# Optimization experiments

Measured on AMD Instinct MI355X. Metric: run time of the kernel, lower is better.

Reference implementation:

```python
import jax, jax.numpy as jnp
import numpy as np

B, T, D, H = 256, 512, 512, 512


def setup_inputs() -> dict:
    key = jax.random.key(0)
    k1, k2, k3, k4 = jax.random.split(key, 4)
    inputs = jax.random.normal(k1, (B, T, D), dtype=jnp.float32)
    lengths = jax.random.randint(k2, (B,), 0, T).astype(jnp.int32)
    # LSTM params. Flax nn.LSTMCell uses per-gate dense layers:
    #  input dense (with bias) and recurrent dense (no bias). Packing the
    #  four gates (i, f, g, o) into one matrix is mathematically identical.
    Wx = jax.random.normal(k3, (D, 4 * H), dtype=jnp.float32) * (1.0 / np.sqrt(D))
    Wh = jax.random.normal(k4, (H, 4 * H), dtype=jnp.float32) * (1.0 / np.sqrt(H))
    b = jnp.zeros((4 * H,), dtype=jnp.float32)
    return {"inputs": inputs, "lengths": lengths, "Wx": Wx, "Wh": Wh, "b": b}


def reference(inputs, lengths, Wx, Wh, b):
    batch = inputs.shape[0]
    hidden = Wh.shape[0]
    x_tbd = jnp.swapaxes(inputs, 0, 1)  # [T, B, D]

    def step(carry, x_t):
        c, h = carry
        # fused gate pre-activations: [B, 4H]
        z = x_t @ Wx + h @ Wh + b
        i, f, g, o = jnp.split(z, 4, axis=-1)
        i = jax.nn.sigmoid(i)
        f = jax.nn.sigmoid(f)
        g = jnp.tanh(g)
        o = jax.nn.sigmoid(o)
        c_new = f * c + i * g
        h_new = o * jnp.tanh(c_new)
        return (c_new, h_new), h_new

    c0 = jnp.zeros((batch, hidden), dtype=inputs.dtype)
    h0 = jnp.zeros((batch, hidden), dtype=inputs.dtype)
    _, hs = jax.lax.scan(step, (c0, h0), x_tbd)  # hs: [T, B, H]

    # select output at last valid timestep per example
    idx = jnp.maximum(0, lengths - 1)  # [B]
    return hs[idx, jnp.arange(batch), :]  # [B, H]
```

## Files before the change

### kernel.cpp

```cpp
#include <hip/hip_runtime.h>

#define Bb 256
#define Tt 512
#define Dd 512
#define Hh 512
#define KTOT 1024
#define FOURH 2048

typedef __attribute__((ext_vector_type(8))) short bf16x8;
typedef __attribute__((ext_vector_type(4))) float f32x4;

__device__ __forceinline__ unsigned short f2bf(float f) {
    union { float f; unsigned u; } x; x.f = f;
    unsigned u = x.u;
    unsigned r = u + 0x7FFFu + ((u >> 16) & 1u);
    return (unsigned short)(r >> 16);
}
__device__ __forceinline__ float bf2f(unsigned short s) {
    union { unsigned u; float f; } x; x.u = ((unsigned)s) << 16;
    return x.f;
}

__device__ __forceinline__ uint4 load16_sc0(const void* p) {
    uint4 v;
    asm volatile("global_load_dwordx4 %0, %1, off sc0" : "=v"(v) : "v"(p));
    return v;
}
__device__ __forceinline__ uint4 load16_sc01(const void* p) {
    uint4 v;
    asm volatile("global_load_dwordx4 %0, %1, off sc0 sc1" : "=v"(v) : "v"(p));
    return v;
}

__global__ void prep_w(const float* __restrict__ Wx, const float* __restrict__ Wh,
                       unsigned short* __restrict__ WT_hi, unsigned short* __restrict__ WT_lo) {
    __shared__ float tile[32][33];
    int n0 = (blockIdx.x & 63) * 32;
    int k0 = (blockIdx.x >> 6) * 32;
    int tx = threadIdx.x & 31;
    int ty = threadIdx.x >> 5;
    for (int q = 0; q < 4; ++q) {
        int k = k0 + ty + q * 8;
        int n = n0 + tx;
        float v = (k < Dd) ? Wx[(size_t)k * FOURH + n] : Wh[(size_t)(k - Dd) * FOURH + n];
        tile[ty + q * 8][tx] = v;
    }
    __syncthreads();
    for (int q = 0; q < 4; ++q) {
        int nl = ty + q * 8;
        int kl = tx;
        float v = tile[kl][nl];
        unsigned short hi = f2bf(v);
        unsigned short lo = f2bf(v - bf2f(hi));
        size_t o = (size_t)(n0 + nl) * KTOT + (size_t)(k0 + kl);
        WT_hi[o] = hi;
        WT_lo[o] = lo;
    }
}

__global__ void init_state(float* __restrict__ c_st,
                           unsigned short* __restrict__ h_bufs,
                           unsigned int* __restrict__ ctrl) {
    int i = blockIdx.x * blockDim.x + threadIdx.x;
    if (i < Bb * Hh) {
        c_st[i] = 0.f;
        for (int q = 0; q < 4; ++q)
            h_bufs[(size_t)q * Bb * Hh + i] = 0;
    }
    if (i < 272) ctrl[i] = 0u;
}

__global__ __launch_bounds__(512) void lstm_persist5(
    const float* __restrict__ X, const int* __restrict__ lengths,
    const unsigned short* __restrict__ WT_hi, const unsigned short* __restrict__ WT_lo,
    const float* __restrict__ bias,
    unsigned short* __restrict__ h_base,
    unsigned int* __restrict__ ctrl,
    float* __restrict__ out)
{
    __shared__ unsigned short HLDS[32768];
    __shared__ unsigned short XLDS[32768];
    __shared__ float zbuf[8][32][17];
    __shared__ int sgrp, sslt, smix;

    const int tid = threadIdx.x;
    const int w8 = tid >> 6;
    const int lane = tid & 63;
    const int l15 = lane & 15;
    const int q4 = lane >> 4;
    const int klo = q4 * 8;

    unsigned xcc;
    asm volatile("s_getreg_b32 %0, hwreg(HW_REG_XCC_ID, 0, 4)" : "=s"(xcc));
    xcc &= 7u;

    unsigned int* pool = ctrl + 256;
    unsigned int* rcnt = ctrl + 264;

    if (tid == 0) {
        unsigned my = __hip_atomic_fetch_add(&pool[xcc], 1u, __ATOMIC_RELAXED, __HIP_MEMORY_SCOPE_SYSTEM);
        asm volatile("s_waitcnt vmcnt(0)" ::: "memory");
        __hip_atomic_fetch_add(rcnt, 1u, __ATOMIC_RELAXED, __HIP_MEMORY_SCOPE_SYSTEM);
        while (__hip_atomic_load(rcnt, __ATOMIC_RELAXED, __HIP_MEMORY_SCOPE_SYSTEM) < 256u)
            __builtin_amdgcn_s_sleep(2);
        unsigned cl[8];
        for (int g = 0; g < 8; ++g)
            cl[g] = __hip_atomic_load(&pool[g], __ATOMIC_RELAXED, __HIP_MEMORY_SCOPE_SYSTEM);
        int group = 0, slot = 0;
        if (my < 32u) { group = (int)xcc; slot = (int)my; }
        else {
            int r = (int)my - 32;
            for (int g = 0; g < (int)xcc; ++g) { int e = (int)cl[g] - 32; if (e > 0) r += e; }
            for (int g = 0; g < 8; ++g) {
                int def = 32 - (int)cl[g];
                if (def <= 0) continue;
                if (r < def) { group = g; slot = (int)cl[g] + r; break; }
                r -= def;
            }
        }
        sgrp = group; sslt = slot; smix = (cl[group] < 32u) ? 1 : 0;
    }
    __syncthreads();
    const int group = sgrp;
    const int slot = sslt;
    const int mixed = smix;

    const int r0 = group * 32;
    const int j0 = slot * 16;
    const int gate = w8 & 3;
    const int khalf = w8 >> 2;

    const size_t HB = (size_t)Bb * Hh;
    unsigned short* h_hi0 = h_base;
    unsigned short* h_lo0 = h_base + HB;
    unsigned short* h_hi1 = h_base + 2 * HB;
    unsigned short* h_lo1 = h_base + 3 * HB;

    const int colg = gate * 512 + j0 + l15;
    const size_t bbase = (size_t)colg * KTOT + (size_t)khalf * 512;
    const unsigned short* bhp = &WT_hi[bbase];
    const unsigned short* blp = &WT_lo[bbase];

    const int xr = tid >> 4;
    const int xk0 = (tid & 15) * 32;
    const float* xbase = &X[((size_t)(r0 + xr) * Tt) * Dd + xk0];

    const int er = tid >> 4;
    const int ej = tid & 15;
    const int row_g = r0 + er;
    const int col_h = j0 + ej;
    const size_t oidx = (size_t)row_g * Hh + col_h;
    int oT = lengths[row_g] - 1; if (oT < 0) oT = 0;
    const float b0 = bias[col_h], b1 = bias[512 + col_h],
                b2 = bias[1024 + col_h], b3 = bias[1536 + col_h];
    float creg = 0.f;

    unsigned int* mycnt = &ctrl[group * 32];

    for (int t = 0; t < Tt; ++t) {
        const unsigned short* hrh = (t & 1) ? h_hi1 : h_hi0;
        const unsigned short* hrl = (t & 1) ? h_lo1 : h_lo0;
        unsigned short* hwh = (t & 1) ? h_hi0 : h_hi1;
        unsigned short* hwl = (t & 1) ? h_lo0 : h_lo1;

        float4 xv[8];
        const float* xp = xbase + (size_t)t * Dd;
#pragma unroll
        for (int i = 0; i < 8; ++i) xv[i] = ((const float4*)xp)[i];

        uint4 hv[8];
        const unsigned short* hsliceh = hrh + (size_t)r0 * Hh;
        const unsigned short* hslicel = hrl + (size_t)r0 * Hh;
        if (!mixed) {
#pragma unroll
            for (int i = 0; i < 8; ++i) {
                const int c = i * 512 + tid;
                const unsigned short* src = ((c >> 11) ? hslicel : hsliceh) + (c & 2047) * 8;
                hv[i] = load16_sc0(src);
            }
        } else {
#pragma unroll
            for (int i = 0; i < 8; ++i) {
                const int c = i * 512 + tid;
                const unsigned short* src = ((c >> 11) ? hslicel : hsliceh) + (c & 2047) * 8;
                hv[i] = load16_sc01(src);
            }
        }
        asm volatile("s_waitcnt vmcnt(0)" ::: "memory");
        __builtin_amdgcn_sched_barrier(0);

#pragma unroll
        for (int i = 0; i < 8; ++i) {
            const int c = i * 512 + tid;
            const int arr = c >> 11, cc = c & 2047;
            const int row = cc >> 6, k8 = cc & 63;
            const int mi = row >> 4, lr = row & 15, ks = k8 >> 2, qq = k8 & 3;
            *(uint4*)&HLDS[((size_t)((arr * 2 + mi) * 16 + ks) * 64 + (qq * 16 + lr)) * 8] = hv[i];
        }
#pragma unroll
        for (int c2 = 0; c2 < 4; ++c2) {
            float vv[8];
            *(float4*)&vv[0] = xv[2 * c2];
            *(float4*)&vv[4] = xv[2 * c2 + 1];
            bf16x8 hv8, lv8;
#pragma unroll
            for (int e = 0; e < 8; ++e) {
                unsigned short hs = f2bf(vv[e]);
                hv8[e] = (short)hs;
                lv8[e] = (short)f2bf(vv[e] - bf2f(hs));
            }
            const int k = xk0 + c2 * 8;
            const int mi = xr >> 4, lr = xr & 15, ks = k >> 5, qq = (k >> 3) & 3;
            const int lidx = ((mi * 16 + ks) * 64 + (qq * 16 + lr)) * 8;
            *(bf16x8*)&XLDS[lidx] = hv8;
            *(bf16x8*)&XLDS[lidx + 16384] = lv8;
        }
        __syncthreads();

        const unsigned short* ALDS = khalf ? HLDS : XLDS;
        f32x4 acc[2][3];
#pragma unroll
        for (int mi = 0; mi < 2; ++mi)
#pragma unroll
            for (int s = 0; s < 3; ++s)
                acc[mi][s] = (f32x4){0.f, 0.f, 0.f, 0.f};

#pragma unroll
        for (int ks = 0; ks < 16; ++ks) {
            const int kk = ks * 32 + klo;
            const bf16x8 bh = *(const bf16x8*)&bhp[kk];
            const bf16x8 bl = *(const bf16x8*)&blp[kk];
#pragma unroll
            for (int mi = 0; mi < 2; ++mi) {
                const bf16x8 ah = *(const bf16x8*)&ALDS[((mi * 16 + ks) * 64 + lane) * 8];
                const bf16x8 al = *(const bf16x8*)&ALDS[(((2 + mi) * 16 + ks) * 64 + lane) * 8];
                acc[mi][0] = __builtin_amdgcn_mfma_f32_16x16x32_bf16(ah, bh, acc[mi][0], 0, 0, 0);
                acc[mi][1] = __builtin_amdgcn_mfma_f32_16x16x32_bf16(ah, bl, acc[mi][1], 0, 0, 0);
                acc[mi][2] = __builtin_amdgcn_mfma_f32_16x16x32_bf16(al, bh, acc[mi][2], 0, 0, 0);
            }
        }

#pragma unroll
        for (int mi = 0; mi < 2; ++mi) {
            const f32x4 z = acc[mi][0] + acc[mi][1] + acc[mi][2];
#pragma unroll
            for (int r = 0; r < 4; ++r)
                zbuf[w8][mi * 16 + q4 * 4 + r][l15] = z[r];
        }
        __syncthreads();

        float zi = zbuf[0][er][ej] + zbuf[4][er][ej] + b0;
        float zf = zbuf[1][er][ej] + zbuf[5][er][ej] + b1;
        float zg = zbuf[2][er][ej] + zbuf[6][er][ej] + b2;
        float zo = zbuf[3][er][ej] + zbuf[7][er][ej] + b3;
        float ig = 1.f / (1.f + expf(-zi));
        float fg = 1.f / (1.f + expf(-zf));
        float gg = tanhf(zg);
        float og = 1.f / (1.f + expf(-zo));
        float cn = fg * creg + ig * gg;
        creg = cn;
        float hn = og * tanhf(cn);
        unsigned short hh = f2bf(hn);
        unsigned short hl = f2bf(hn - bf2f(hh));
        if (!mixed) {
            hwh[oidx] = hh;
            hwl[oidx] = hl;
        } else {
            __hip_atomic_store(&hwh[oidx], hh, __ATOMIC_RELAXED, __HIP_MEMORY_SCOPE_SYSTEM);
            __hip_atomic_store(&hwl[oidx], hl, __ATOMIC_RELAXED, __HIP_MEMORY_SCOPE_SYSTEM);
        }
        if (t == oT) out[oidx] = hn;

        if (t < Tt - 1) {
            __syncthreads();
            if (tid == 0) {
                __hip_atomic_fetch_add(mycnt, 1u, __ATOMIC_RELAXED, __HIP_MEMORY_SCOPE_SYSTEM);
                const unsigned int target = (unsigned int)(t + 1) * 32u;
                while (__hip_atomic_load(mycnt, __ATOMIC_RELAXED, __HIP_MEMORY_SCOPE_SYSTEM) < target)
                    __builtin_amdgcn_s_sleep(2);
            }
            __syncthreads();
        }
    }
}

__global__ __launch_bounds__(512) void lstm_step4(
    const float* __restrict__ X, const int* __restrict__ lengths,
    const unsigned short* __restrict__ WT_hi, const unsigned short* __restrict__ WT_lo,
    const float* __restrict__ bias,
    float* __restrict__ c_st,
    const unsigned short* __restrict__ h_r_hi, const unsigned short* __restrict__ h_r_lo,
    unsigned short* __restrict__ h_w_hi, unsigned short* __restrict__ h_w_lo,
    float* __restrict__ out, int t)
{
    __shared__ float zbuf[8][16][17];

    const int bx = blockIdx.x;
    const int xcd = bx & 7;
    const int rem = bx >> 3;
    const int m0 = (rem & 15) * 16;
    const int col_group = xcd * 4 + (rem >> 4);
    const int hc0 = col_group * 16;
    const int tid = threadIdx.x;
    const int w8 = tid >> 6;
    const int lane = tid & 63;
    const int gate = w8 & 3;
    const int khalf = w8 >> 2;

    f32x4 ahh = (f32x4){0,0,0,0}, ahl = (f32x4){0,0,0,0}, alh = (f32x4){0,0,0,0};

    const int colk = gate * 512 + hc0 + (lane & 15);
    const size_t bbase = (size_t)colk * KTOT;
    const int klo = (lane >> 4) * 8;
    const int row = m0 + (lane & 15);

    if (khalf == 0) {
        const float* xrow = &X[((size_t)row * Tt + t) * Dd];
        const unsigned short* bhp = &WT_hi[bbase];
        const unsigned short* blp = &WT_lo[bbase];
#pragma unroll
        for (int ks = 0; ks < 16; ++ks) {
            const int kk = ks * 32 + klo;
            const float4 v0 = *(const float4*)&xrow[kk];
            const float4 v1 = *(const float4*)&xrow[kk + 4];
            float vv[8] = {v0.x, v0.y, v0.z, v0.w, v1.x, v1.y, v1.z, v1.w};
            bf16x8 ah, al;
#pragma unroll
            for (int e = 0; e < 8; ++e) {
                unsigned short hi = f2bf(vv[e]);
                ah[e] = (short)hi;
                al[e] = (short)f2bf(vv[e] - bf2f(hi));
            }
            const bf16x8 bh = *(const bf16x8*)&bhp[kk];
            const bf16x8 bl = *(const bf16x8*)&blp[kk];
            ahh = __builtin_amdgcn_mfma_f32_16x16x32_bf16(ah, bh, ahh, 0, 0, 0);
            ahl = __builtin_amdgcn_mfma_f32_16x16x32_bf16(ah, bl, ahl, 0, 0, 0);
            alh = __builtin_amdgcn_mfma_f32_16x16x32_bf16(al, bh, alh, 0, 0, 0);
        }
    } else {
        const unsigned short* hrh = &h_r_hi[(size_t)row * Hh];
        const unsigned short* hrl = &h_r_lo[(size_t)row * Hh];
        const unsigned short* bhp = &WT_hi[bbase + 512];
        const unsigned short* blp = &WT_lo[bbase + 512];
#pragma unroll
        for (int ks = 0; ks < 16; ++ks) {
            const int kk = ks * 32 + klo;
            const bf16x8 ah = *(const bf16x8*)&hrh[kk];
            const bf16x8 al = *(const bf16x8*)&hrl[kk];
            const bf16x8 bh = *(const bf16x8*)&bhp[kk];
            const bf16x8 bl = *(const bf16x8*)&blp[kk];
            ahh = __builtin_amdgcn_mfma_f32_16x16x32_bf16(ah, bh, ahh, 0, 0, 0);
            ahl = __builtin_amdgcn_mfma_f32_16x16x32_bf16(ah, bl, ahl, 0, 0, 0);
            alh = __builtin_amdgcn_mfma_f32_16x16x32_bf16(al, bh, alh, 0, 0, 0);
        }
    }

    const f32x4 z = ahh + ahl + alh;
#pragma unroll
    for (int r = 0; r < 4; ++r)
        zbuf[w8][(lane >> 4) * 4 + r][lane & 15] = z[r];
    __syncthreads();

    if (tid < 256) {
        const int r = tid >> 4;
        const int j = tid & 15;
        const int row_g = m0 + r;
        const int col_g = hc0 + j;
        float zi = zbuf[0][r][j] + zbuf[4][r][j] + bias[col_g];
        float zf = zbuf[1][r][j] + zbuf[5][r][j] + bias[512 + col_g];
        float zg = zbuf[2][r][j] + zbuf[6][r][j] + bias[1024 + col_g];
        float zo = zbuf[3][r][j] + zbuf[7][r][j] + bias[1536 + col_g];
        float ig = 1.f / (1.f + expf(-zi));
        float fg = 1.f / (1.f + expf(-zf));
        float gg = tanhf(zg);
        float og = 1.f / (1.f + expf(-zo));
        const size_t idx = (size_t)row_g * Hh + col_g;
        float cn = fg * c_st[idx] + ig * gg;
        float hn = og * tanhf(cn);
        c_st[idx] = cn;
        unsigned short hh = f2bf(hn);
        h_w_hi[idx] = hh;
        h_w_lo[idx] = f2bf(hn - bf2f(hh));
        int len = lengths[row_g];
        int oidx = len - 1; if (oidx < 0) oidx = 0;
        if (t == oidx) out[idx] = hn;
    }
}

extern "C" void kernel_launch(void* const* d_in, const int* in_sizes, int n_in,
                              void* d_out, int out_size, void* d_ws, size_t ws_size,
                              hipStream_t stream) {
    const float* X = (const float*)d_in[0];
    const int* lengths = (const int*)d_in[1];
    const float* Wx = (const float*)d_in[2];
    const float* Wh = (const float*)d_in[3];
    const float* bias = (const float*)d_in[4];
    float* out = (float*)d_out;

    char* ws = (char*)d_ws;
    unsigned short* WT_hi = (unsigned short*)ws;
    unsigned short* WT_lo = (unsigned short*)(ws + (4u << 20));
    float* c_st = (float*)(ws + (8u << 20));
    unsigned short* h_base = (unsigned short*)(ws + (8u << 20) + (512u << 10));
    unsigned int* ctrl = (unsigned int*)(ws + (8u << 20) + (1536u << 10));
    const size_t HB = (size_t)Bb * Hh;
    unsigned short* h_hi0 = h_base;
    unsigned short* h_lo0 = h_base + HB;
    unsigned short* h_hi1 = h_base + 2 * HB;
    unsigned short* h_lo1 = h_base + 3 * HB;

    hipLaunchKernelGGL(prep_w, dim3(2048), dim3(256), 0, stream, Wx, Wh, WT_hi, WT_lo);
    hipLaunchKernelGGL(init_state, dim3(512), dim3(256), 0, stream, c_st, h_base, ctrl);

    void* args[] = { (void*)&X, (void*)&lengths, (void*)&WT_hi, (void*)&WT_lo,
                     (void*)&bias, (void*)&h_base, (void*)&ctrl, (void*)&out };
    hipError_t err = hipLaunchCooperativeKernel((const void*)lstm_persist5,
                                                dim3(256), dim3(512), args, 0, stream);
    if (err != hipSuccess) {
        for (int t = 0; t < Tt; ++t) {
            const bool even = (t & 1) == 0;
            hipLaunchKernelGGL(lstm_step4, dim3(512), dim3(512), 0, stream,
                               X, lengths, WT_hi, WT_lo, bias, c_st,
                               even ? h_hi0 : h_hi1, even ? h_lo0 : h_lo1,
                               even ? h_hi1 : h_hi0, even ? h_lo1 : h_lo0,
                               out, t);
        }
    }
}
```

Baseline: 7.551 ms.

## Use static block mapping with packed h state and global grid barrier

Drops the dynamic XCC-aware group assignment and per-group 32-block barriers. Each block now takes a fixed row/column tile from blockIdx, and all 256 blocks sync through one global counter every timestep. The hi/lo bf16 halves of h are packed into one 32-bit word, so each step issues fewer atomic stores and loads. XOR swizzling is added to the LDS layouts to cut bank conflicts. The cost is a heavier all-block barrier, since each block now needs h from every column owner, and h reads move into system-scope atomic loads.

```diff
diff --git a/kernel.cpp b/kernel.cpp
--- a/kernel.cpp
+++ b/kernel.cpp
@@ -19,17 +19,6 @@
 __device__ __forceinline__ float bf2f(unsigned short s) {
     union { unsigned u; float f; } x; x.u = ((unsigned)s) << 16;
     return x.f;
-}
-
-__device__ __forceinline__ uint4 load16_sc0(const void* p) {
-    uint4 v;
-    asm volatile("global_load_dwordx4 %0, %1, off sc0" : "=v"(v) : "v"(p));
-    return v;
-}
-__device__ __forceinline__ uint4 load16_sc01(const void* p) {
-    uint4 v;
-    asm volatile("global_load_dwordx4 %0, %1, off sc0 sc1" : "=v"(v) : "v"(p));
-    return v;
 }
 
 __global__ void prep_w(const float* __restrict__ Wx, const float* __restrict__ Wh,
@@ -58,85 +47,47 @@
     }
 }
 
-__global__ void init_state(float* __restrict__ c_st,
-                           unsigned short* __restrict__ h_bufs,
-                           unsigned int* __restrict__ ctrl) {
-    int i = blockIdx.x * blockDim.x + threadIdx.x;
-    if (i < Bb * Hh) {
-        c_st[i] = 0.f;
-        for (int q = 0; q < 4; ++q)
-            h_bufs[(size_t)q * Bb * Hh + i] = 0;
-    }
-    if (i < 272) ctrl[i] = 0u;
-}
-
-__global__ __launch_bounds__(512) void lstm_persist5(
+__global__ void init_state3(char* __restrict__ ws, int persist) {
+    long i = (long)blockIdx.x * blockDim.x + threadIdx.x;
+    if (i < 98304) {
+        *(uint4*)(ws + (8u << 20) + i * 16) = (uint4){0, 0, 0, 0};
+    }
+    if (persist && i < 64) {
+        ((unsigned int*)(ws + (8u << 20) + (1536u << 10)))[i] = 0u;
+    }
+}
+
+__global__ __launch_bounds__(512) void lstm_persist7(
     const float* __restrict__ X, const int* __restrict__ lengths,
     const unsigned short* __restrict__ WT_hi, const unsigned short* __restrict__ WT_lo,
     const float* __restrict__ bias,
-    unsigned short* __restrict__ h_base,
+    unsigned int* __restrict__ h_pack,
     unsigned int* __restrict__ ctrl,
     float* __restrict__ out)
 {
     __shared__ unsigned short HLDS[32768];
     __shared__ unsigned short XLDS[32768];
     __shared__ float zbuf[8][32][17];
-    __shared__ int sgrp, sslt, smix;
-
+
+    const int bx = blockIdx.x;
+    const int group = bx & 7;
+    const int slot = bx >> 3;
+    const int rt = slot & 7;
+    const int cs = slot >> 3;
+    const int r0 = rt * 32;
+    const int j0h = group * 64 + cs * 16;
     const int tid = threadIdx.x;
     const int w8 = tid >> 6;
     const int lane = tid & 63;
     const int l15 = lane & 15;
     const int q4 = lane >> 4;
     const int klo = q4 * 8;
-
-    unsigned xcc;
-    asm volatile("s_getreg_b32 %0, hwreg(HW_REG_XCC_ID, 0, 4)" : "=s"(xcc));
-    xcc &= 7u;
-
-    unsigned int* pool = ctrl + 256;
-    unsigned int* rcnt = ctrl + 264;
-
-    if (tid == 0) {
-        unsigned my = __hip_atomic_fetch_add(&pool[xcc], 1u, __ATOMIC_RELAXED, __HIP_MEMORY_SCOPE_SYSTEM);
-        asm volatile("s_waitcnt vmcnt(0)" ::: "memory");
-        __hip_atomic_fetch_add(rcnt, 1u, __ATOMIC_RELAXED, __HIP_MEMORY_SCOPE_SYSTEM);
-        while (__hip_atomic_load(rcnt, __ATOMIC_RELAXED, __HIP_MEMORY_SCOPE_SYSTEM) < 256u)
-            __builtin_amdgcn_s_sleep(2);
-        unsigned cl[8];
-        for (int g = 0; g < 8; ++g)
-            cl[g] = __hip_atomic_load(&pool[g], __ATOMIC_RELAXED, __HIP_MEMORY_SCOPE_SYSTEM);
-        int group = 0, slot = 0;
-        if (my < 32u) { group = (int)xcc; slot = (int)my; }
-        else {
-            int r = (int)my - 32;
-            for (int g = 0; g < (int)xcc; ++g) { int e = (int)cl[g] - 32; if (e > 0) r += e; }
-            for (int g = 0; g < 8; ++g) {
-                int def = 32 - (int)cl[g];
-                if (def <= 0) continue;
-                if (r < def) { group = g; slot = (int)cl[g] + r; break; }
-                r -= def;
-            }
-        }
-        sgrp = group; sslt = slot; smix = (cl[group] < 32u) ? 1 : 0;
-    }
-    __syncthreads();
-    const int group = sgrp;
-    const int slot = sslt;
-    const int mixed = smix;
-
-    const int r0 = group * 32;
-    const int j0 = slot * 16;
     const int gate = w8 & 3;
     const int khalf = w8 >> 2;
 
     const size_t HB = (size_t)Bb * Hh;
-    unsigned short* h_hi0 = h_base;
-    unsigned short* h_lo0 = h_base + HB;
-    unsigned short* h_hi1 = h_base + 2 * HB;
-    unsigned short* h_lo1 = h_base + 3 * HB;
-
-    const int colg = gate * 512 + j0 + l15;
+
+    const int colg = gate * 512 + j0h + l15;
     const size_t bbase = (size_t)colg * KTOT + (size_t)khalf * 512;
     const unsigned short* bhp = &WT_hi[bbase];
     const unsigned short* blp = &WT_lo[bbase];
@@ -148,72 +99,79 @@
     const int er = tid >> 4;
     const int ej = tid & 15;
     const int row_g = r0 + er;
-    const int col_h = j0 + ej;
+    const int col_h = j0h + ej;
     const size_t oidx = (size_t)row_g * Hh + col_h;
     int oT = lengths[row_g] - 1; if (oT < 0) oT = 0;
     const float b0 = bias[col_h], b1 = bias[512 + col_h],
                 b2 = bias[1024 + col_h], b3 = bias[1536 + col_h];
     float creg = 0.f;
 
-    unsigned int* mycnt = &ctrl[group * 32];
+    unsigned int* gcnt = ctrl;
 
     for (int t = 0; t < Tt; ++t) {
-        const unsigned short* hrh = (t & 1) ? h_hi1 : h_hi0;
-        const unsigned short* hrl = (t & 1) ? h_lo1 : h_lo0;
-        unsigned short* hwh = (t & 1) ? h_hi0 : h_hi1;
-        unsigned short* hwl = (t & 1) ? h_lo0 : h_lo1;
-
-        float4 xv[8];
-        const float* xp = xbase + (size_t)t * Dd;
-#pragma unroll
-        for (int i = 0; i < 8; ++i) xv[i] = ((const float4*)xp)[i];
-
-        uint4 hv[8];
-        const unsigned short* hsliceh = hrh + (size_t)r0 * Hh;
-        const unsigned short* hslicel = hrl + (size_t)r0 * Hh;
-        if (!mixed) {
-#pragma unroll
-            for (int i = 0; i < 8; ++i) {
-                const int c = i * 512 + tid;
-                const unsigned short* src = ((c >> 11) ? hslicel : hsliceh) + (c & 2047) * 8;
-                hv[i] = load16_sc0(src);
+        const int p_r = t & 1;
+        const unsigned int* hp_r = h_pack + (size_t)p_r * HB;
+        unsigned int* hp_w = h_pack + (size_t)(p_r ^ 1) * HB;
+
+        unsigned long long hq[16];
+#pragma unroll
+        for (int it = 0; it < 4; ++it) {
+            const int c = it * 512 + tid;
+            const int row = c >> 6, k8 = c & 63;
+            const unsigned long long* p =
+                (const unsigned long long*)(hp_r + ((size_t)(r0 + row) * Hh + k8 * 8));
+#pragma unroll
+            for (int j = 0; j < 4; ++j)
+                hq[it * 4 + j] = __hip_atomic_load(p + j, __ATOMIC_RELAXED, __HIP_MEMORY_SCOPE_SYSTEM);
+        }
+
+        {
+            const float* xp = xbase + (size_t)t * Dd;
+            float4 xv[8];
+#pragma unroll
+            for (int i = 0; i < 8; ++i) xv[i] = ((const float4*)xp)[i];
+            const int ksx = tid & 15;
+            const int mi = xr >> 4, lr = xr & 15;
+#pragma unroll
+            for (int c2 = 0; c2 < 4; ++c2) {
+                float vv[8];
+                *(float4*)&vv[0] = xv[2 * c2];
+                *(float4*)&vv[4] = xv[2 * c2 + 1];
+                bf16x8 hv8, lv8;
+#pragma unroll
+                for (int e = 0; e < 8; ++e) {
+                    unsigned short hs = f2bf(vv[e]);
+                    hv8[e] = (short)hs;
+                    lv8[e] = (short)f2bf(vv[e] - bf2f(hs));
+                }
+                const int lnw = (c2 * 16 + lr) ^ (ksx & 7);
+                *(bf16x8*)&XLDS[(((0 * 2 + mi) * 16 + ksx) * 64 + lnw) * 8] = hv8;
+                *(bf16x8*)&XLDS[(((1 * 2 + mi) * 16 + ksx) * 64 + lnw) * 8] = lv8;
             }
-        } else {
-#pragma unroll
-            for (int i = 0; i < 8; ++i) {
-                const int c = i * 512 + tid;
-                const unsigned short* src = ((c >> 11) ? hslicel : hsliceh) + (c & 2047) * 8;
-                hv[i] = load16_sc01(src);
-            }
-        }
-        asm volatile("s_waitcnt vmcnt(0)" ::: "memory");
-        __builtin_amdgcn_sched_barrier(0);
-
-#pragma unroll
-        for (int i = 0; i < 8; ++i) {
-            const int c = i * 512 + tid;
-            const int arr = c >> 11, cc = c & 2047;
-            const int row = cc >> 6, k8 = cc & 63;
-            const int mi = row >> 4, lr = row & 15, ks = k8 >> 2, qq = k8 & 3;
-            *(uint4*)&HLDS[((size_t)((arr * 2 + mi) * 16 + ks) * 64 + (qq * 16 + lr)) * 8] = hv[i];
-        }
-#pragma unroll
-        for (int c2 = 0; c2 < 4; ++c2) {
-            float vv[8];
-            *(float4*)&vv[0] = xv[2 * c2];
-            *(float4*)&vv[4] = xv[2 * c2 + 1];
-            bf16x8 hv8, lv8;
-#pragma unroll
-            for (int e = 0; e < 8; ++e) {
-                unsigned short hs = f2bf(vv[e]);
-                hv8[e] = (short)hs;
-                lv8[e] = (short)f2bf(vv[e] - bf2f(hs));
-            }
-            const int k = xk0 + c2 * 8;
-            const int mi = xr >> 4, lr = xr & 15, ks = k >> 5, qq = (k >> 3) & 3;
-            const int lidx = ((mi * 16 + ks) * 64 + (qq * 16 + lr)) * 8;
-            *(bf16x8*)&XLDS[lidx] = hv8;
-            *(bf16x8*)&XLDS[lidx + 16384] = lv8;
+        }
+
+#pragma unroll
+        for (int it = 0; it < 4; ++it) {
+            const int c = it * 512 + tid;
+            const int row = c >> 6, k8 = c & 63;
+            const int ksh = k8 >> 2, qq = k8 & 3;
+            const int mi = row >> 4, lr = row & 15;
+            const unsigned int u0 = (unsigned int)hq[it * 4 + 0], u1 = (unsigned int)(hq[it * 4 + 0] >> 32);
+            const unsigned int u2 = (unsigned int)hq[it * 4 + 1], u3 = (unsigned int)(hq[it * 4 + 1] >> 32);
+            const unsigned int u4 = (unsigned int)hq[it * 4 + 2], u5 = (unsigned int)(hq[it * 4 + 2] >> 32);
+            const unsigned int u6 = (unsigned int)hq[it * 4 + 3], u7 = (unsigned int)(hq[it * 4 + 3] >> 32);
+            uint4 hiw, low;
+            hiw.x = (u0 >> 16) | (u1 & 0xffff0000u);
+            hiw.y = (u2 >> 16) | (u3 & 0xffff0000u);
+            hiw.z = (u4 >> 16) | (u5 & 0xffff0000u);
+            hiw.w = (u6 >> 16) | (u7 & 0xffff0000u);
+            low.x = (u0 & 0xffffu) | (u1 << 16);
+            low.y = (u2 & 0xffffu) | (u3 << 16);
+            low.z = (u4 & 0xffffu) | (u5 << 16);
+            low.w = (u6 & 0xffffu) | (u7 << 16);
+            const int lnw = (qq * 16 + lr) ^ (ksh & 7);
+            *(uint4*)&HLDS[(((0 * 2 + mi) * 16 + ksh) * 64 + lnw) * 8] = hiw;
+            *(uint4*)&HLDS[(((1 * 2 + mi) * 16 + ksh) * 64 + lnw) * 8] = low;
         }
         __syncthreads();
 
@@ -230,10 +188,11 @@
             const int kk = ks * 32 + klo;
             const bf16x8 bh = *(const bf16x8*)&bhp[kk];
             const bf16x8 bl = *(const bf16x8*)&blp[kk];
+            const int lnr = lane ^ (ks & 7);
 #pragma unroll
             for (int mi = 0; mi < 2; ++mi) {
-                const bf16x8 ah = *(const bf16x8*)&ALDS[((mi * 16 + ks) * 64 + lane) * 8];
-                const bf16x8 al = *(const bf16x8*)&ALDS[(((2 + mi) * 16 + ks) * 64 + lane) * 8];
+                const bf16x8 ah = *(const bf16x8*)&ALDS[(((0 * 2 + mi) * 16 + ks) * 64 + lnr) * 8];
+                const bf16x8 al = *(const bf16x8*)&ALDS[(((1 * 2 + mi) * 16 + ks) * 64 + lnr) * 8];
                 acc[mi][0] = __builtin_amdgcn_mfma_f32_16x16x32_bf16(ah, bh, acc[mi][0], 0, 0, 0);
                 acc[mi][1] = __builtin_amdgcn_mfma_f32_16x16x32_bf16(ah, bl, acc[mi][1], 0, 0, 0);
                 acc[mi][2] = __builtin_amdgcn_mfma_f32_16x16x32_bf16(al, bh, acc[mi][2], 0, 0, 0);
@@ -262,22 +221,18 @@
         float hn = og * tanhf(cn);
         unsigned short hh = f2bf(hn);
         unsigned short hl = f2bf(hn - bf2f(hh));
-        if (!mixed) {
-            hwh[oidx] = hh;
-            hwl[oidx] = hl;
-        } else {
-            __hip_atomic_store(&hwh[oidx], hh, __ATOMIC_RELAXED, __HIP_MEMORY_SCOPE_SYSTEM);
-            __hip_atomic_store(&hwl[oidx], hl, __ATOMIC_RELAXED, __HIP_MEMORY_SCOPE_SYSTEM);
-        }
+        unsigned int up = ((unsigned int)hh << 16) | (unsigned int)hl;
+        __hip_atomic_store(&hp_w[oidx], up, __ATOMIC_RELAXED, __HIP_MEMORY_SCOPE_SYSTEM);
         if (t == oT) out[oidx] = hn;
 
         if (t < Tt - 1) {
+            asm volatile("s_waitcnt vmcnt(0)" ::: "memory");
             __syncthreads();
             if (tid == 0) {
-                __hip_atomic_fetch_add(mycnt, 1u, __ATOMIC_RELAXED, __HIP_MEMORY_SCOPE_SYSTEM);
-                const unsigned int target = (unsigned int)(t + 1) * 32u;
-                while (__hip_atomic_load(mycnt, __ATOMIC_RELAXED, __HIP_MEMORY_SCOPE_SYSTEM) < target)
-                    __builtin_amdgcn_s_sleep(2);
+                __hip_atomic_fetch_add(gcnt, 1u, __ATOMIC_RELAXED, __HIP_MEMORY_SCOPE_SYSTEM);
+                const unsigned int tgt = (unsigned int)(t + 1) * 256u;
+                while (__hip_atomic_load(gcnt, __ATOMIC_RELAXED, __HIP_MEMORY_SCOPE_SYSTEM) < tgt)
+                    __builtin_amdgcn_s_sleep(4);
             }
             __syncthreads();
         }
@@ -400,22 +355,29 @@
     char* ws = (char*)d_ws;
     unsigned short* WT_hi = (unsigned short*)ws;
     unsigned short* WT_lo = (unsigned short*)(ws + (4u << 20));
+    unsigned int* h_pack = (unsigned int*)(ws + (8u << 20));
+    unsigned int* ctrl = (unsigned int*)(ws + (8u << 20) + (1536u << 10));
     float* c_st = (float*)(ws + (8u << 20));
     unsigned short* h_base = (unsigned short*)(ws + (8u << 20) + (512u << 10));
-    unsigned int* ctrl = (unsigned int*)(ws + (8u << 20) + (1536u << 10));
     const size_t HB = (size_t)Bb * Hh;
     unsigned short* h_hi0 = h_base;
     unsigned short* h_lo0 = h_base + HB;
     unsigned short* h_hi1 = h_base + 2 * HB;
     unsigned short* h_lo1 = h_base + 3 * HB;
 
+    const size_t NEED_PERSIST = (8u << 20) + (1536u << 10) + 4096u;
+    const int can_persist = (ws_size >= NEED_PERSIST) ? 1 : 0;
+
     hipLaunchKernelGGL(prep_w, dim3(2048), dim3(256), 0, stream, Wx, Wh, WT_hi, WT_lo);
-    hipLaunchKernelGGL(init_state, dim3(512), dim3(256), 0, stream, c_st, h_base, ctrl);
-
-    void* args[] = { (void*)&X, (void*)&lengths, (void*)&WT_hi, (void*)&WT_lo,
-                     (void*)&bias, (void*)&h_base, (void*)&ctrl, (void*)&out };
-    hipError_t err = hipLaunchCooperativeKernel((const void*)lstm_persist5,
-                                                dim3(256), dim3(512), args, 0, stream);
+    hipLaunchKernelGGL(init_state3, dim3(512), dim3(256), 0, stream, ws, can_persist);
+
+    hipError_t err = hipErrorUnknown;
+    if (can_persist) {
+        void* args[] = { (void*)&X, (void*)&lengths, (void*)&WT_hi, (void*)&WT_lo,
+                         (void*)&bias, (void*)&h_pack, (void*)&ctrl, (void*)&out };
+        err = hipLaunchCooperativeKernel((const void*)lstm_persist7,
+                                         dim3(256), dim3(512), args, 0, stream);
+    }
     if (err != hipSuccess) {
         for (int t = 0; t < Tt; ++t) {
             const bool even = (t & 1) == 0;
```

New measurement: 7.873 ms. 4.3% more time.
